# Kernel tuning notes

Hardware: AMD Instinct MI355X
Metric: run time of the kernel (lower is better)

## Reference

```python
import jax, jax.numpy as jnp
import numpy as np

N_GRAPHS = 20
NUM_GENES = 5000
N = N_GRAPHS * NUM_GENES
E = 1_600_000
F_IN = 64
H = 64
EMB = 64
L = 3  # num message-passing layers
SLOPE = 0.01  # LeakyReLU negative slope (torch default)
BN_EPS = 1e-5


def setup_inputs() -> dict:
    key = jax.random.key(0)
    ks = jax.random.split(key, 16)
    s = lambda *shape: 0.05  # init scale
    inp = {
        "x": jax.random.normal(ks[0], (N, F_IN), dtype=jnp.float32),
        "edge_index": jax.random.randint(ks[1], (2, E), 0, N, dtype=jnp.int64),
        "pre_w": jax.random.normal(ks[2], (F_IN, H), dtype=jnp.float32) * 0.05,
        "pre_b": jnp.zeros((H,), jnp.float32),
        "conv_w1": jax.random.normal(ks[3], (L, H, H), dtype=jnp.float32) * 0.05,
        "conv_b1": jnp.zeros((L, H), jnp.float32),
        "conv_w2": jax.random.normal(ks[4], (L, H, H), dtype=jnp.float32) * 0.05,
        "conv_b2": jnp.zeros((L, H), jnp.float32),
        "bn_g": jnp.ones((L - 1, H), jnp.float32),
        "bn_b": jnp.zeros((L - 1, H), jnp.float32),
        "post_w1": jax.random.normal(ks[5], (H, H), dtype=jnp.float32) * 0.05,
        "post_b1": jnp.zeros((H,), jnp.float32),
        "post_w2": jax.random.normal(ks[6], (H, EMB), dtype=jnp.float32) * 0.05,
        "post_b2": jnp.zeros((EMB,), jnp.float32),
    }
    return inp


def _gin_conv(h, src, dst, w1, b1, w2, b2):
    # GINConv(eps=0): mlp(x + sum_{j in N(i)} x_j)
    agg = jax.ops.segment_sum(h[src], dst, num_segments=N)  # [N, H]
    z = h + agg
    z = jax.nn.leaky_relu(z @ w1 + b1, negative_slope=SLOPE)
    return z @ w2 + b2


def _batchnorm(h, g, b):
    mu = jnp.mean(h, axis=0)
    var = jnp.var(h, axis=0)
    return (h - mu) * jax.lax.rsqrt(var + BN_EPS) * g + b


def reference(x, edge_index, pre_w, pre_b, conv_w1, conv_b1, conv_w2, conv_b2,
              bn_g, bn_b, post_w1, post_b1, post_w2, post_b2):
    src, dst = edge_index[0], edge_index[1]
    h = x @ pre_w + pre_b
    for l in range(L - 1):
        h = _gin_conv(h, src, dst, conv_w1[l], conv_b1[l], conv_w2[l], conv_b2[l])
        h = _batchnorm(h, bn_g[l], bn_b[l])
    h = _gin_conv(h, src, dst, conv_w1[L - 1], conv_b1[L - 1], conv_w2[L - 1], conv_b2[L - 1])
    h = jax.nn.leaky_relu(h @ post_w1 + post_b1, negative_slope=SLOPE)
    h = h @ post_w2 + post_b2  # [N, EMB]
    return h.reshape(N_GRAPHS, NUM_GENES * EMB)
```

## Files before the change

kernel.cpp:

```cpp
#include <hip/hip_runtime.h>
#include <hip/hip_bf16.h>

#define NN 100000
#define EE 1600000
#define HD 64
#define SLOPE 0.01f
#define BN_EPS 1e-5f
#define TS_BF 144
#define TS_F32 272

#define BSHIFT 9
#define BSIZE 512
#define NBUCK ((NN + BSIZE - 1) / BSIZE)
#define BCAP 16384
#define CHUNKE 8192
#define NBLKA ((EE + CHUNKE - 1) / CHUNKE)

typedef __attribute__((ext_vector_type(8))) short short8;
typedef __attribute__((ext_vector_type(8))) __bf16 bf16x8;
typedef __attribute__((ext_vector_type(4))) float f32x4;

__device__ __forceinline__ float lrelu(float v) { return v > 0.f ? v : SLOPE * v; }
__device__ __forceinline__ float bflo(unsigned u) { return __uint_as_float(u << 16); }
__device__ __forceinline__ float bfhi(unsigned u) { return __uint_as_float(u & 0xFFFF0000u); }
__device__ __forceinline__ unsigned short f2bf(float f) {
    __hip_bfloat16 hb = __float2bfloat16(f);
    return *reinterpret_cast<unsigned short*>(&hb);
}

__global__ __launch_bounds__(256) void k_binit(int* __restrict__ bcursor) {
    int t = threadIdx.x;
    if (t < NBUCK) bcursor[t] = t * BCAP;
}

__global__ __launch_bounds__(256) void k_bucketa(const int* __restrict__ src,
                                                 const int* __restrict__ dst,
                                                 int* __restrict__ bcursor,
                                                 int* __restrict__ staging) {
    __shared__ int hist[NBUCK], base_l[NBUCK], cur_l[NBUCK];
    int tid = threadIdx.x;
    int base = blockIdx.x * CHUNKE;
    int nE = min(CHUNKE, EE - base);
    for (int i = tid; i < NBUCK; i += 256) hist[i] = 0;
    __syncthreads();
    for (int k = tid; k < nE; k += 256)
        atomicAdd(&hist[dst[base + k] >> BSHIFT], 1);
    __syncthreads();
    for (int i = tid; i < NBUCK; i += 256) {
        int h = hist[i];
        base_l[i] = h ? atomicAdd(&bcursor[i], h) : 0;
        cur_l[i] = 0;
    }
    __syncthreads();
    for (int k = tid; k < nE; k += 256) {
        int d = dst[base + k];
        int s = src[base + k];
        int b = d >> BSHIFT;
        int off = atomicAdd(&cur_l[b], 1);
        staging[base_l[b] + off] = (s << BSHIFT) | (d & (BSIZE - 1));
    }
}

__global__ __launch_bounds__(256) void k_bscan(const int* __restrict__ bcursor,
                                               int* __restrict__ bbase,
                                               int* __restrict__ row_ptr) {
    __shared__ int sc[256], cnt[256];
    int tid = threadIdx.x;
    int c = (tid < NBUCK) ? (bcursor[tid] - tid * BCAP) : 0;
    cnt[tid] = c;
    sc[tid] = c;
    __syncthreads();
    for (int s = 1; s < 256; s <<= 1) {
        int v = (tid >= s) ? sc[tid - s] : 0;
        __syncthreads();
        sc[tid] += v;
        __syncthreads();
    }
    if (tid < NBUCK) bbase[tid] = sc[tid] - cnt[tid];
    if (tid == 0) row_ptr[NN] = EE;
}

__global__ __launch_bounds__(256) void k_bucketb(const int* __restrict__ staging,
                                                 const int* __restrict__ bcursor,
                                                 const int* __restrict__ bbase,
                                                 int* __restrict__ row_ptr,
                                                 int* __restrict__ csr) {
    __shared__ int cnt[BSIZE], sc[BSIZE], cur[BSIZE];
    int b = blockIdx.x, tid = threadIdx.x;
    int cnt_e = bcursor[b] - b * BCAP;
    int sbase = b * BCAP;
    int n0 = b * BSIZE;
    int nn = min(BSIZE, NN - n0);
    int bb = bbase[b];
    cnt[tid] = 0;
    cnt[tid + 256] = 0;
    __syncthreads();
    for (int i = tid; i < cnt_e; i += 256)
        atomicAdd(&cnt[staging[sbase + i] & (BSIZE - 1)], 1);
    __syncthreads();
    sc[tid] = cnt[tid];
    sc[tid + 256] = cnt[tid + 256];
    __syncthreads();
    for (int s = 1; s < BSIZE; s <<= 1) {
        int i0 = tid, i1 = tid + 256;
        int v0 = (i0 >= s) ? sc[i0 - s] : 0;
        int v1 = (i1 >= s) ? sc[i1 - s] : 0;
        __syncthreads();
        sc[i0] += v0;
        sc[i1] += v1;
        __syncthreads();
    }
    int e0 = sc[tid] - cnt[tid];
    int e1 = sc[tid + 256] - cnt[tid + 256];
    cur[tid] = e0;
    cur[tid + 256] = e1;
    if (tid < nn) row_ptr[n0 + tid] = bb + e0;
    if (tid + 256 < nn) row_ptr[n0 + tid + 256] = bb + e1;
    __syncthreads();
    for (int i = tid; i < cnt_e; i += 256) {
        int v = staging[sbase + i];
        int off = atomicAdd(&cur[v & (BSIZE - 1)], 1);
        csr[bb + off] = v >> BSHIFT;
    }
}

__global__ __launch_bounds__(256) void k_packw(const float* __restrict__ pre_w,
                                               const float* __restrict__ conv_w1,
                                               const float* __restrict__ conv_w2,
                                               const float* __restrict__ post_w1,
                                               const float* __restrict__ post_w2,
                                               unsigned short* __restrict__ wp) {
    int g = blockIdx.x >> 1;
    int c = (blockIdx.x & 1) * 256 + threadIdx.x;
    const float* W;
    switch (g) {
        case 0: W = pre_w; break;
        case 1: W = conv_w1; break;
        case 2: W = conv_w2; break;
        case 3: W = conv_w1 + 4096; break;
        case 4: W = conv_w2 + 4096; break;
        case 5: W = conv_w1 + 8192; break;
        case 6: W = conv_w2 + 8192; break;
        case 7: W = post_w1; break;
        default: W = post_w2; break;
    }
    int nt = c >> 7, ks = (c >> 6) & 1, ln = c & 63;
    int n = nt * 16 + (ln & 15);
    unsigned short* dstp = wp + (size_t)g * 4096 + (size_t)c * 8;
#pragma unroll
    for (int j = 0; j < 8; j++) {
        int k = ks * 32 + (ln >> 4) * 8 + j;
        dstp[j] = f2bf(W[k * HD + n]);
    }
}

__global__ __launch_bounds__(256, 4) void k_pre(const float* __restrict__ x,
                                                const unsigned short* __restrict__ wp0,
                                                const float* __restrict__ bias,
                                                unsigned short* __restrict__ h) {
    __shared__ char lds_all[4][16 * TS_BF];
    int tid = threadIdx.x, lane = tid & 63, wid = tid >> 6;
    int lg = lane >> 4, li = lane & 15;
    char* base = lds_all[wid];

    bf16x8 wf[4][2];
#pragma unroll
    for (int nt = 0; nt < 4; nt++)
#pragma unroll
        for (int ks = 0; ks < 2; ks++)
            wf[nt][ks] = __builtin_bit_cast(bf16x8,
                *(const short8*)(wp0 + ((size_t)((nt * 2 + ks) * 64 + lane)) * 8));
    float bb[4];
#pragma unroll
    for (int nt = 0; nt < 4; nt++) bb[nt] = bias[nt * 16 + li];

    int gwave = (blockIdx.x * 256 + tid) >> 6;
    int nwaves = (gridDim.x * 256) >> 6;
    for (int tile = gwave; tile < NN / 16; tile += nwaves) {
        int row = tile * 16 + li;
        bf16x8 af[2];
#pragma unroll
        for (int ks = 0; ks < 2; ks++) {
            const float* p = x + (size_t)row * HD + ks * 32 + lg * 8;
            union { unsigned short u[8]; short8 s; } t;
#pragma unroll
            for (int j = 0; j < 8; j++) t.u[j] = f2bf(p[j]);
            af[ks] = __builtin_bit_cast(bf16x8, t.s);
        }
        f32x4 acc[4];
#pragma unroll
        for (int nt = 0; nt < 4; nt++) acc[nt] = (f32x4){0.f, 0.f, 0.f, 0.f};
#pragma unroll
        for (int ks = 0; ks < 2; ks++)
#pragma unroll
            for (int nt = 0; nt < 4; nt++)
                acc[nt] = __builtin_amdgcn_mfma_f32_16x16x32_bf16(af[ks], wf[nt][ks], acc[nt], 0, 0, 0);
#pragma unroll
        for (int nt = 0; nt < 4; nt++)
#pragma unroll
            for (int r = 0; r < 4; r++)
                *(unsigned short*)(base + (lg * 4 + r) * TS_BF + (nt * 16 + li) * 2)
                    = f2bf(acc[nt][r] + bb[nt]);
#pragma unroll
        for (int s = 0; s < 2; s++) {
            short8 t = *(short8*)(base + li * TS_BF + (s * 4 + lg) * 16);
            *(short8*)(h + (size_t)row * HD + (s * 4 + lg) * 8) = t;
        }
    }
}

template<bool OUTF32, bool STATS>
__global__ __launch_bounds__(256, 3) void k_fmlp(const unsigned short* __restrict__ in,
                                                 const unsigned short* __restrict__ wpa,
                                                 const unsigned short* __restrict__ wpb,
                                                 const float* __restrict__ b1,
                                                 const float* __restrict__ b2,
                                                 void* __restrict__ outp,
                                                 float* __restrict__ stats_out) {
    __shared__ char lds_all[4][16 * TS_F32];
    int tid = threadIdx.x, lane = tid & 63, wid = tid >> 6;
    int lg = lane >> 4, li = lane & 15;
    char* base = lds_all[wid];

    bf16x8 w1f[4][2], w2f[4][2];
#pragma unroll
    for (int nt = 0; nt < 4; nt++)
#pragma unroll
        for (int ks = 0; ks < 2; ks++) {
            w1f[nt][ks] = __builtin_bit_cast(bf16x8,
                *(const short8*)(wpa + ((size_t)((nt * 2 + ks) * 64 + lane)) * 8));
            w2f[nt][ks] = __builtin_bit_cast(bf16x8,
                *(const short8*)(wpb + ((size_t)((nt * 2 + ks) * 64 + lane)) * 8));
        }
    float bb1[4], bb2[4];
#pragma unroll
    for (int nt = 0; nt < 4; nt++) {
        bb1[nt] = b1[nt * 16 + li];
        bb2[nt] = b2[nt * 16 + li];
    }

    float s1[4] = {0.f, 0.f, 0.f, 0.f}, s2[4] = {0.f, 0.f, 0.f, 0.f};
    int gwave = (blockIdx.x * 256 + tid) >> 6;
    int nwaves = (gridDim.x * 256) >> 6;
    for (int tile = gwave; tile < NN / 16; tile += nwaves) {
        int row = tile * 16 + li;
        bf16x8 af[2];
#pragma unroll
        for (int ks = 0; ks < 2; ks++)
            af[ks] = __builtin_bit_cast(bf16x8,
                *(const short8*)(in + (size_t)row * HD + ks * 32 + lg * 8));
        f32x4 acc[4];
#pragma unroll
        for (int nt = 0; nt < 4; nt++) acc[nt] = (f32x4){0.f, 0.f, 0.f, 0.f};
#pragma unroll
        for (int ks = 0; ks < 2; ks++)
#pragma unroll
            for (int nt = 0; nt < 4; nt++)
                acc[nt] = __builtin_amdgcn_mfma_f32_16x16x32_bf16(af[ks], w1f[nt][ks], acc[nt], 0, 0, 0);
#pragma unroll
        for (int nt = 0; nt < 4; nt++)
#pragma unroll
            for (int r = 0; r < 4; r++)
                *(unsigned short*)(base + (lg * 4 + r) * TS_BF + (nt * 16 + li) * 2)
                    = f2bf(lrelu(acc[nt][r] + bb1[nt]));
        bf16x8 a2[2];
#pragma unroll
        for (int ks = 0; ks < 2; ks++)
            a2[ks] = *(bf16x8*)(base + li * TS_BF + (ks * 32 + lg * 8) * 2);
        f32x4 acc2[4];
#pragma unroll
        for (int nt = 0; nt < 4; nt++) acc2[nt] = (f32x4){0.f, 0.f, 0.f, 0.f};
#pragma unroll
        for (int ks = 0; ks < 2; ks++)
#pragma unroll
            for (int nt = 0; nt < 4; nt++)
                acc2[nt] = __builtin_amdgcn_mfma_f32_16x16x32_bf16(a2[ks], w2f[nt][ks], acc2[nt], 0, 0, 0);
        if (OUTF32) {
#pragma unroll
            for (int nt = 0; nt < 4; nt++)
#pragma unroll
                for (int r = 0; r < 4; r++)
                    *(float*)(base + (lg * 4 + r) * TS_F32 + (nt * 16 + li) * 4)
                        = acc2[nt][r] + bb2[nt];
#pragma unroll
            for (int s = 0; s < 4; s++) {
                f32x4 t = *(f32x4*)(base + li * TS_F32 + (s * 4 + lg) * 16);
                *(f32x4*)((float*)outp + (size_t)row * HD + (s * 4 + lg) * 4) = t;
            }
        } else {
#pragma unroll
            for (int nt = 0; nt < 4; nt++) {
#pragma unroll
                for (int r = 0; r < 4; r++) {
                    float u = acc2[nt][r] + bb2[nt];
                    if (STATS) { s1[nt] += u; s2[nt] += u * u; }
                    *(unsigned short*)(base + (lg * 4 + r) * TS_BF + (nt * 16 + li) * 2)
                        = f2bf(u);
                }
            }
#pragma unroll
            for (int s = 0; s < 2; s++) {
                short8 t = *(short8*)(base + li * TS_BF + (s * 4 + lg) * 16);
                *(short8*)((unsigned short*)outp + (size_t)row * HD + (s * 4 + lg) * 8) = t;
            }
        }
    }
    if (STATS) {
#pragma unroll
        for (int nt = 0; nt < 4; nt++) {
            float a = s1[nt], b = s2[nt];
            a += __shfl_xor(a, 16); a += __shfl_xor(a, 32);
            b += __shfl_xor(b, 16); b += __shfl_xor(b, 32);
            if (lg == 0) {
                atomicAdd(&stats_out[nt * 16 + li], a);
                atomicAdd(&stats_out[64 + nt * 16 + li], b);
            }
        }
    }
}

__global__ __launch_bounds__(256, 6) void k_gather(const unsigned short* __restrict__ h,
                                                   const int* __restrict__ row_ptr,
                                                   const int* __restrict__ csr,
                                                   const float* __restrict__ bn_stats,
                                                   const float* __restrict__ bn_g,
                                                   const float* __restrict__ bn_b,
                                                   int apply_bn,
                                                   unsigned short* __restrict__ z) {
    int tid = threadIdx.x;
    int lane = tid & 63;
    int g = lane >> 4;
    int fq = lane & 15;
    int wave = (blockIdx.x * 256 + tid) >> 6;
    int node = wave * 4 + g;
    if (node >= NN) return;

    float sc[4] = {1.f, 1.f, 1.f, 1.f}, sh[4] = {0.f, 0.f, 0.f, 0.f};
    if (apply_bn) {
        float inv = 1.f / (float)NN;
#pragma unroll
        for (int j = 0; j < 4; j++) {
            int f = fq * 4 + j;
            float mu = bn_stats[f] * inv;
            float var = bn_stats[64 + f] * inv - mu * mu;
            float s = rsqrtf(var + BN_EPS) * bn_g[f];
            sc[j] = s;
            sh[j] = bn_b[f] - mu * s;
        }
    }

    const uint2* hv = (const uint2*)h;
    int r0 = row_ptr[node], re = row_ptr[node + 1];
    uint2 sv = hv[(size_t)node * 16 + fq];
    float a0[4], a1[4] = {0, 0, 0, 0}, a2[4] = {0, 0, 0, 0}, a3[4] = {0, 0, 0, 0};
    a0[0] = bflo(sv.x); a0[1] = bfhi(sv.x); a0[2] = bflo(sv.y); a0[3] = bfhi(sv.y);

    int e = r0;
    for (; e + 8 <= re; e += 8) {
        int i0 = csr[e], i1 = csr[e + 1], i2 = csr[e + 2], i3 = csr[e + 3];
        int i4 = csr[e + 4], i5 = csr[e + 5], i6 = csr[e + 6], i7 = csr[e + 7];
        uint2 v0 = hv[(size_t)i0 * 16 + fq];
        uint2 v1 = hv[(size_t)i1 * 16 + fq];
        uint2 v2 = hv[(size_t)i2 * 16 + fq];
        uint2 v3 = hv[(size_t)i3 * 16 + fq];
        uint2 v4 = hv[(size_t)i4 * 16 + fq];
        uint2 v5 = hv[(size_t)i5 * 16 + fq];
        uint2 v6 = hv[(size_t)i6 * 16 + fq];
        uint2 v7 = hv[(size_t)i7 * 16 + fq];
        a0[0] += bflo(v0.x); a0[1] += bfhi(v0.x); a0[2] += bflo(v0.y); a0[3] += bfhi(v0.y);
        a1[0] += bflo(v1.x); a1[1] += bfhi(v1.x); a1[2] += bflo(v1.y); a1[3] += bfhi(v1.y);
        a2[0] += bflo(v2.x); a2[1] += bfhi(v2.x); a2[2] += bflo(v2.y); a2[3] += bfhi(v2.y);
        a3[0] += bflo(v3.x); a3[1] += bfhi(v3.x); a3[2] += bflo(v3.y); a3[3] += bfhi(v3.y);
        a0[0] += bflo(v4.x); a0[1] += bfhi(v4.x); a0[2] += bflo(v4.y); a0[3] += bfhi(v4.y);
        a1[0] += bflo(v5.x); a1[1] += bfhi(v5.x); a1[2] += bflo(v5.y); a1[3] += bfhi(v5.y);
        a2[0] += bflo(v6.x); a2[1] += bfhi(v6.x); a2[2] += bflo(v6.y); a2[3] += bfhi(v6.y);
        a3[0] += bflo(v7.x); a3[1] += bfhi(v7.x); a3[2] += bflo(v7.y); a3[3] += bfhi(v7.y);
    }
    for (; e < re; e++) {
        uint2 v = hv[(size_t)csr[e] * 16 + fq];
        a0[0] += bflo(v.x); a0[1] += bfhi(v.x); a0[2] += bflo(v.y); a0[3] += bfhi(v.y);
    }
    float cnt = (float)(re - r0 + 1);
    unsigned short o[4];
#pragma unroll
    for (int j = 0; j < 4; j++) {
        float s = ((a0[j] + a1[j]) + (a2[j] + a3[j]));
        if (apply_bn) s = fmaf(s, sc[j], cnt * sh[j]);
        o[j] = f2bf(s);
    }
    uint2 ov;
    ov.x = (unsigned)o[0] | ((unsigned)o[1] << 16);
    ov.y = (unsigned)o[2] | ((unsigned)o[3] << 16);
    ((uint2*)z)[(size_t)node * 16 + fq] = ov;
}

extern "C" void kernel_launch(void* const* d_in, const int* in_sizes, int n_in,
                              void* d_out, int out_size, void* d_ws, size_t ws_size,
                              hipStream_t stream) {
    const float* x = (const float*)d_in[0];
    const int* edge = (const int*)d_in[1];
    const float* pre_w = (const float*)d_in[2];
    const float* pre_b = (const float*)d_in[3];
    const float* conv_w1 = (const float*)d_in[4];
    const float* conv_b1 = (const float*)d_in[5];
    const float* conv_w2 = (const float*)d_in[6];
    const float* conv_b2 = (const float*)d_in[7];
    const float* bn_g = (const float*)d_in[8];
    const float* bn_b = (const float*)d_in[9];
    const float* post_w1 = (const float*)d_in[10];
    const float* post_b1 = (const float*)d_in[11];
    const float* post_w2 = (const float*)d_in[12];
    const float* post_b2 = (const float*)d_in[13];
    float* out = (float*)d_out;

    const int* src = edge;
    const int* dst = edge + EE;

    unsigned short* hH = (unsigned short*)d_ws;
    unsigned short* zZ = hH + (size_t)NN * HD;
    float* stats0 = (float*)(zZ + (size_t)NN * HD);
    float* stats1 = stats0 + 128;
    unsigned short* wp = (unsigned short*)(stats1 + 128);
    int* row_ptr = (int*)(wp + 9 * 4096);
    int* csr = row_ptr + NN + 4;
    int* bcursor = csr + EE;
    int* bbase = bcursor + 256;
    int* staging = bbase + 256;

    dim3 blk(256);
    dim3 gG(6250), gM(782);

    hipMemsetAsync(stats0, 0, 256 * sizeof(float), stream);
    hipLaunchKernelGGL(k_binit, dim3(1), blk, 0, stream, bcursor);
    hipLaunchKernelGGL(k_bucketa, dim3(NBLKA), blk, 0, stream, src, dst, bcursor, staging);
    hipLaunchKernelGGL(k_bscan, dim3(1), blk, 0, stream, bcursor, bbase, row_ptr);
    hipLaunchKernelGGL(k_bucketb, dim3(NBUCK), blk, 0, stream, staging, bcursor, bbase,
                       row_ptr, csr);

    hipLaunchKernelGGL(k_packw, dim3(18), blk, 0, stream,
                       pre_w, conv_w1, conv_w2, post_w1, post_w2, wp);

    hipLaunchKernelGGL(k_pre, gM, blk, 0, stream, x, wp + 0 * 4096, pre_b, hH);

    hipLaunchKernelGGL(k_gather, gG, blk, 0, stream, hH, row_ptr, csr,
                       (const float*)nullptr, (const float*)nullptr, (const float*)nullptr, 0, zZ);
    hipLaunchKernelGGL((k_fmlp<false, true>), gM, blk, 0, stream, zZ,
                       wp + 1 * 4096, wp + 2 * 4096, conv_b1, conv_b2, (void*)hH, stats0);

    hipLaunchKernelGGL(k_gather, gG, blk, 0, stream, hH, row_ptr, csr,
                       stats0, bn_g, bn_b, 1, zZ);
    hipLaunchKernelGGL((k_fmlp<false, true>), gM, blk, 0, stream, zZ,
                       wp + 3 * 4096, wp + 4 * 4096, conv_b1 + HD, conv_b2 + HD, (void*)hH, stats1);

    hipLaunchKernelGGL(k_gather, gG, blk, 0, stream, hH, row_ptr, csr,
                       stats1, bn_g + HD, bn_b + HD, 1, zZ);
    hipLaunchKernelGGL((k_fmlp<false, false>), gM, blk, 0, stream, zZ,
                       wp + 5 * 4096, wp + 6 * 4096, conv_b1 + 2 * HD, conv_b2 + 2 * HD,
                       (void*)hH, stats0);

    hipLaunchKernelGGL((k_fmlp<true, false>), gM, blk, 0, stream, hH,
                       wp + 7 * 4096, wp + 8 * 4096, post_b1, post_b2, (void*)out, stats0);
}
```

Before: 375.4 us.

## Fuse neighbor gather with GIN MLP into a single per-tile kernel

Merges the edge-gather aggregation (with BatchNorm folding) and the two-layer GIN MLP into one kernel, where each wave gathers 16 nodes into LDS and then runs the MFMA MLP on them. This removes the intermediate z buffer round-trip through global memory and three kernel launches. Ping-pong buffers replace the in-place h/z pair, and the post MLP is split into its own kernel. The trade-off is fewer concurrent waves for the latency-bound gather and heavier register use per wave.

```diff
diff --git a/kernel.cpp b/kernel.cpp
--- a/kernel.cpp
+++ b/kernel.cpp
@@ -8,6 +8,7 @@
 #define BN_EPS 1e-5f
 #define TS_BF 144
 #define TS_F32 272
+#define NTILE (NN / 16)
 
 #define BSHIFT 9
 #define BSIZE 512
@@ -176,7 +177,7 @@
 
     int gwave = (blockIdx.x * 256 + tid) >> 6;
     int nwaves = (gridDim.x * 256) >> 6;
-    for (int tile = gwave; tile < NN / 16; tile += nwaves) {
+    for (int tile = gwave; tile < NTILE; tile += nwaves) {
         int row = tile * 16 + li;
         bf16x8 af[2];
 #pragma unroll
@@ -209,18 +210,26 @@
     }
 }
 
-template<bool OUTF32, bool STATS>
-__global__ __launch_bounds__(256, 3) void k_fmlp(const unsigned short* __restrict__ in,
-                                                 const unsigned short* __restrict__ wpa,
-                                                 const unsigned short* __restrict__ wpb,
-                                                 const float* __restrict__ b1,
-                                                 const float* __restrict__ b2,
-                                                 void* __restrict__ outp,
-                                                 float* __restrict__ stats_out) {
-    __shared__ char lds_all[4][16 * TS_F32];
+template<bool APPLY_BN, bool STATS>
+__global__ __launch_bounds__(256, 4) void k_gfmlp(const unsigned short* __restrict__ h,
+                                                  const int* __restrict__ row_ptr,
+                                                  const int* __restrict__ csr,
+                                                  const float* __restrict__ bn_stats,
+                                                  const float* __restrict__ bn_g,
+                                                  const float* __restrict__ bn_b,
+                                                  const unsigned short* __restrict__ wpa,
+                                                  const unsigned short* __restrict__ wpb,
+                                                  const float* __restrict__ b1,
+                                                  const float* __restrict__ b2,
+                                                  unsigned short* __restrict__ outp,
+                                                  float* __restrict__ stats_out) {
+    __shared__ char lds_all[4][16 * TS_BF];
     int tid = threadIdx.x, lane = tid & 63, wid = tid >> 6;
     int lg = lane >> 4, li = lane & 15;
     char* base = lds_all[wid];
+
+    int tile = (blockIdx.x * 256 + tid) >> 6;
+    if (tile >= NTILE) return;
 
     bf16x8 w1f[4][2], w2f[4][2];
 #pragma unroll
@@ -239,71 +248,113 @@
         bb2[nt] = b2[nt * 16 + li];
     }
 
+    float sc[4], sh[4];
+    if (APPLY_BN) {
+        float inv = 1.f / (float)NN;
+#pragma unroll
+        for (int j = 0; j < 4; j++) {
+            int f = li * 4 + j;
+            float mu = bn_stats[f] * inv;
+            float var = bn_stats[64 + f] * inv - mu * mu;
+            float s = rsqrtf(var + BN_EPS) * bn_g[f];
+            sc[j] = s;
+            sh[j] = bn_b[f] - mu * s;
+        }
+    }
+
+    const uint2* hv = (const uint2*)h;
+#pragma unroll
+    for (int b = 0; b < 4; b++) {
+        int node = tile * 16 + b * 4 + lg;
+        int r0 = row_ptr[node], re = row_ptr[node + 1];
+        uint2 sv = hv[(size_t)node * 16 + li];
+        float a0[4], a1[4] = {0, 0, 0, 0}, a2[4] = {0, 0, 0, 0}, a3[4] = {0, 0, 0, 0};
+        a0[0] = bflo(sv.x); a0[1] = bfhi(sv.x); a0[2] = bflo(sv.y); a0[3] = bfhi(sv.y);
+        int e = r0;
+        for (; e + 8 <= re; e += 8) {
+            int i0 = csr[e], i1 = csr[e + 1], i2 = csr[e + 2], i3 = csr[e + 3];
+            int i4 = csr[e + 4], i5 = csr[e + 5], i6 = csr[e + 6], i7 = csr[e + 7];
+            uint2 v0 = hv[(size_t)i0 * 16 + li];
+            uint2 v1 = hv[(size_t)i1 * 16 + li];
+            uint2 v2 = hv[(size_t)i2 * 16 + li];
+            uint2 v3 = hv[(size_t)i3 * 16 + li];
+            uint2 v4 = hv[(size_t)i4 * 16 + li];
+            uint2 v5 = hv[(size_t)i5 * 16 + li];
+            uint2 v6 = hv[(size_t)i6 * 16 + li];
+            uint2 v7 = hv[(size_t)i7 * 16 + li];
+            a0[0] += bflo(v0.x); a0[1] += bfhi(v0.x); a0[2] += bflo(v0.y); a0[3] += bfhi(v0.y);
+            a1[0] += bflo(v1.x); a1[1] += bfhi(v1.x); a1[2] += bflo(v1.y); a1[3] += bfhi(v1.y);
+            a2[0] += bflo(v2.x); a2[1] += bfhi(v2.x); a2[2] += bflo(v2.y); a2[3] += bfhi(v2.y);
+            a3[0] += bflo(v3.x); a3[1] += bfhi(v3.x); a3[2] += bflo(v3.y); a3[3] += bfhi(v3.y);
+            a0[0] += bflo(v4.x); a0[1] += bfhi(v4.x); a0[2] += bflo(v4.y); a0[3] += bfhi(v4.y);
+            a1[0] += bflo(v5.x); a1[1] += bfhi(v5.x); a1[2] += bflo(v5.y); a1[3] += bfhi(v5.y);
+            a2[0] += bflo(v6.x); a2[1] += bfhi(v6.x); a2[2] += bflo(v6.y); a2[3] += bfhi(v6.y);
+            a3[0] += bflo(v7.x); a3[1] += bfhi(v7.x); a3[2] += bflo(v7.y); a3[3] += bfhi(v7.y);
+        }
+        for (; e < re; e++) {
+            uint2 v = hv[(size_t)csr[e] * 16 + li];
+            a0[0] += bflo(v.x); a0[1] += bfhi(v.x); a0[2] += bflo(v.y); a0[3] += bfhi(v.y);
+        }
+        float cnt = (float)(re - r0 + 1);
+        unsigned short o[4];
+#pragma unroll
+        for (int j = 0; j < 4; j++) {
+            float s = ((a0[j] + a1[j]) + (a2[j] + a3[j]));
+            if (APPLY_BN) s = fmaf(s, sc[j], cnt * sh[j]);
+            o[j] = f2bf(s);
+        }
+        uint2 ov;
+        ov.x = (unsigned)o[0] | ((unsigned)o[1] << 16);
+        ov.y = (unsigned)o[2] | ((unsigned)o[3] << 16);
+        *(uint2*)(base + (b * 4 + lg) * TS_BF + li * 8) = ov;
+    }
+
+    bf16x8 af[2];
+#pragma unroll
+    for (int ks = 0; ks < 2; ks++)
+        af[ks] = *(bf16x8*)(base + li * TS_BF + (ks * 32 + lg * 8) * 2);
+    f32x4 acc[4];
+#pragma unroll
+    for (int nt = 0; nt < 4; nt++) acc[nt] = (f32x4){0.f, 0.f, 0.f, 0.f};
+#pragma unroll
+    for (int ks = 0; ks < 2; ks++)
+#pragma unroll
+        for (int nt = 0; nt < 4; nt++)
+            acc[nt] = __builtin_amdgcn_mfma_f32_16x16x32_bf16(af[ks], w1f[nt][ks], acc[nt], 0, 0, 0);
+#pragma unroll
+    for (int nt = 0; nt < 4; nt++)
+#pragma unroll
+        for (int r = 0; r < 4; r++)
+            *(unsigned short*)(base + (lg * 4 + r) * TS_BF + (nt * 16 + li) * 2)
+                = f2bf(lrelu(acc[nt][r] + bb1[nt]));
+    bf16x8 a2f[2];
+#pragma unroll
+    for (int ks = 0; ks < 2; ks++)
+        a2f[ks] = *(bf16x8*)(base + li * TS_BF + (ks * 32 + lg * 8) * 2);
+    f32x4 acc2[4];
+#pragma unroll
+    for (int nt = 0; nt < 4; nt++) acc2[nt] = (f32x4){0.f, 0.f, 0.f, 0.f};
+#pragma unroll
+    for (int ks = 0; ks < 2; ks++)
+#pragma unroll
+        for (int nt = 0; nt < 4; nt++)
+            acc2[nt] = __builtin_amdgcn_mfma_f32_16x16x32_bf16(a2f[ks], w2f[nt][ks], acc2[nt], 0, 0, 0);
+
     float s1[4] = {0.f, 0.f, 0.f, 0.f}, s2[4] = {0.f, 0.f, 0.f, 0.f};
-    int gwave = (blockIdx.x * 256 + tid) >> 6;
-    int nwaves = (gridDim.x * 256) >> 6;
-    for (int tile = gwave; tile < NN / 16; tile += nwaves) {
-        int row = tile * 16 + li;
-        bf16x8 af[2];
-#pragma unroll
-        for (int ks = 0; ks < 2; ks++)
-            af[ks] = __builtin_bit_cast(bf16x8,
-                *(const short8*)(in + (size_t)row * HD + ks * 32 + lg * 8));
-        f32x4 acc[4];
-#pragma unroll
-        for (int nt = 0; nt < 4; nt++) acc[nt] = (f32x4){0.f, 0.f, 0.f, 0.f};
-#pragma unroll
-        for (int ks = 0; ks < 2; ks++)
-#pragma unroll
-            for (int nt = 0; nt < 4; nt++)
-                acc[nt] = __builtin_amdgcn_mfma_f32_16x16x32_bf16(af[ks], w1f[nt][ks], acc[nt], 0, 0, 0);
-#pragma unroll
-        for (int nt = 0; nt < 4; nt++)
-#pragma unroll
-            for (int r = 0; r < 4; r++)
-                *(unsigned short*)(base + (lg * 4 + r) * TS_BF + (nt * 16 + li) * 2)
-                    = f2bf(lrelu(acc[nt][r] + bb1[nt]));
-        bf16x8 a2[2];
-#pragma unroll
-        for (int ks = 0; ks < 2; ks++)
-            a2[ks] = *(bf16x8*)(base + li * TS_BF + (ks * 32 + lg * 8) * 2);
-        f32x4 acc2[4];
-#pragma unroll
-        for (int nt = 0; nt < 4; nt++) acc2[nt] = (f32x4){0.f, 0.f, 0.f, 0.f};
-#pragma unroll
-        for (int ks = 0; ks < 2; ks++)
-#pragma unroll
-            for (int nt = 0; nt < 4; nt++)
-                acc2[nt] = __builtin_amdgcn_mfma_f32_16x16x32_bf16(a2[ks], w2f[nt][ks], acc2[nt], 0, 0, 0);
-        if (OUTF32) {
-#pragma unroll
-            for (int nt = 0; nt < 4; nt++)
-#pragma unroll
-                for (int r = 0; r < 4; r++)
-                    *(float*)(base + (lg * 4 + r) * TS_F32 + (nt * 16 + li) * 4)
-                        = acc2[nt][r] + bb2[nt];
-#pragma unroll
-            for (int s = 0; s < 4; s++) {
-                f32x4 t = *(f32x4*)(base + li * TS_F32 + (s * 4 + lg) * 16);
-                *(f32x4*)((float*)outp + (size_t)row * HD + (s * 4 + lg) * 4) = t;
-            }
-        } else {
-#pragma unroll
-            for (int nt = 0; nt < 4; nt++) {
-#pragma unroll
-                for (int r = 0; r < 4; r++) {
-                    float u = acc2[nt][r] + bb2[nt];
-                    if (STATS) { s1[nt] += u; s2[nt] += u * u; }
-                    *(unsigned short*)(base + (lg * 4 + r) * TS_BF + (nt * 16 + li) * 2)
-                        = f2bf(u);
-                }
-            }
-#pragma unroll
-            for (int s = 0; s < 2; s++) {
-                short8 t = *(short8*)(base + li * TS_BF + (s * 4 + lg) * 16);
-                *(short8*)((unsigned short*)outp + (size_t)row * HD + (s * 4 + lg) * 8) = t;
-            }
-        }
+#pragma unroll
+    for (int nt = 0; nt < 4; nt++) {
+#pragma unroll
+        for (int r = 0; r < 4; r++) {
+            float u = acc2[nt][r] + bb2[nt];
+            if (STATS) { s1[nt] += u; s2[nt] += u * u; }
+            *(unsigned short*)(base + (lg * 4 + r) * TS_BF + (nt * 16 + li) * 2) = f2bf(u);
+        }
+    }
+    int row = tile * 16 + li;
+#pragma unroll
+    for (int s = 0; s < 2; s++) {
+        short8 t = *(short8*)(base + li * TS_BF + (s * 4 + lg) * 16);
+        *(short8*)(outp + (size_t)row * HD + (s * 4 + lg) * 8) = t;
     }
     if (STATS) {
 #pragma unroll
@@ -319,79 +370,81 @@
     }
 }
 
-__global__ __launch_bounds__(256, 6) void k_gather(const unsigned short* __restrict__ h,
-                                                   const int* __restrict__ row_ptr,
-                                                   const int* __restrict__ csr,
-                                                   const float* __restrict__ bn_stats,
-                                                   const float* __restrict__ bn_g,
-                                                   const float* __restrict__ bn_b,
-                                                   int apply_bn,
-                                                   unsigned short* __restrict__ z) {
-    int tid = threadIdx.x;
-    int lane = tid & 63;
-    int g = lane >> 4;
-    int fq = lane & 15;
-    int wave = (blockIdx.x * 256 + tid) >> 6;
-    int node = wave * 4 + g;
-    if (node >= NN) return;
-
-    float sc[4] = {1.f, 1.f, 1.f, 1.f}, sh[4] = {0.f, 0.f, 0.f, 0.f};
-    if (apply_bn) {
-        float inv = 1.f / (float)NN;
-#pragma unroll
-        for (int j = 0; j < 4; j++) {
-            int f = fq * 4 + j;
-            float mu = bn_stats[f] * inv;
-            float var = bn_stats[64 + f] * inv - mu * mu;
-            float s = rsqrtf(var + BN_EPS) * bn_g[f];
-            sc[j] = s;
-            sh[j] = bn_b[f] - mu * s;
-        }
-    }
-
-    const uint2* hv = (const uint2*)h;
-    int r0 = row_ptr[node], re = row_ptr[node + 1];
-    uint2 sv = hv[(size_t)node * 16 + fq];
-    float a0[4], a1[4] = {0, 0, 0, 0}, a2[4] = {0, 0, 0, 0}, a3[4] = {0, 0, 0, 0};
-    a0[0] = bflo(sv.x); a0[1] = bfhi(sv.x); a0[2] = bflo(sv.y); a0[3] = bfhi(sv.y);
-
-    int e = r0;
-    for (; e + 8 <= re; e += 8) {
-        int i0 = csr[e], i1 = csr[e + 1], i2 = csr[e + 2], i3 = csr[e + 3];
-        int i4 = csr[e + 4], i5 = csr[e + 5], i6 = csr[e + 6], i7 = csr[e + 7];
-        uint2 v0 = hv[(size_t)i0 * 16 + fq];
-        uint2 v1 = hv[(size_t)i1 * 16 + fq];
-        uint2 v2 = hv[(size_t)i2 * 16 + fq];
-        uint2 v3 = hv[(size_t)i3 * 16 + fq];
-        uint2 v4 = hv[(size_t)i4 * 16 + fq];
-        uint2 v5 = hv[(size_t)i5 * 16 + fq];
-        uint2 v6 = hv[(size_t)i6 * 16 + fq];
-        uint2 v7 = hv[(size_t)i7 * 16 + fq];
-        a0[0] += bflo(v0.x); a0[1] += bfhi(v0.x); a0[2] += bflo(v0.y); a0[3] += bfhi(v0.y);
-        a1[0] += bflo(v1.x); a1[1] += bfhi(v1.x); a1[2] += bflo(v1.y); a1[3] += bfhi(v1.y);
-        a2[0] += bflo(v2.x); a2[1] += bfhi(v2.x); a2[2] += bflo(v2.y); a2[3] += bfhi(v2.y);
-        a3[0] += bflo(v3.x); a3[1] += bfhi(v3.x); a3[2] += bflo(v3.y); a3[3] += bfhi(v3.y);
-        a0[0] += bflo(v4.x); a0[1] += bfhi(v4.x); a0[2] += bflo(v4.y); a0[3] += bfhi(v4.y);
-        a1[0] += bflo(v5.x); a1[1] += bfhi(v5.x); a1[2] += bflo(v5.y); a1[3] += bfhi(v5.y);
-        a2[0] += bflo(v6.x); a2[1] += bfhi(v6.x); a2[2] += bflo(v6.y); a2[3] += bfhi(v6.y);
-        a3[0] += bflo(v7.x); a3[1] += bfhi(v7.x); a3[2] += bflo(v7.y); a3[3] += bfhi(v7.y);
-    }
-    for (; e < re; e++) {
-        uint2 v = hv[(size_t)csr[e] * 16 + fq];
-        a0[0] += bflo(v.x); a0[1] += bfhi(v.x); a0[2] += bflo(v.y); a0[3] += bfhi(v.y);
-    }
-    float cnt = (float)(re - r0 + 1);
-    unsigned short o[4];
-#pragma unroll
-    for (int j = 0; j < 4; j++) {
-        float s = ((a0[j] + a1[j]) + (a2[j] + a3[j]));
-        if (apply_bn) s = fmaf(s, sc[j], cnt * sh[j]);
-        o[j] = f2bf(s);
-    }
-    uint2 ov;
-    ov.x = (unsigned)o[0] | ((unsigned)o[1] << 16);
-    ov.y = (unsigned)o[2] | ((unsigned)o[3] << 16);
-    ((uint2*)z)[(size_t)node * 16 + fq] = ov;
+__global__ __launch_bounds__(256, 3) void k_post(const unsigned short* __restrict__ in,
+                                                 const unsigned short* __restrict__ wpa,
+                                                 const unsigned short* __restrict__ wpb,
+                                                 const float* __restrict__ b1,
+                                                 const float* __restrict__ b2,
+                                                 float* __restrict__ outp) {
+    __shared__ char lds_all[4][16 * TS_F32];
+    int tid = threadIdx.x, lane = tid & 63, wid = tid >> 6;
+    int lg = lane >> 4, li = lane & 15;
+    char* base = lds_all[wid];
+
+    bf16x8 w1f[4][2], w2f[4][2];
+#pragma unroll
+    for (int nt = 0; nt < 4; nt++)
+#pragma unroll
+        for (int ks = 0; ks < 2; ks++) {
+            w1f[nt][ks] = __builtin_bit_cast(bf16x8,
+                *(const short8*)(wpa + ((size_t)((nt * 2 + ks) * 64 + lane)) * 8));
+            w2f[nt][ks] = __builtin_bit_cast(bf16x8,
+                *(const short8*)(wpb + ((size_t)((nt * 2 + ks) * 64 + lane)) * 8));
+        }
+    float bb1[4], bb2[4];
+#pragma unroll
+    for (int nt = 0; nt < 4; nt++) {
+        bb1[nt] = b1[nt * 16 + li];
+        bb2[nt] = b2[nt * 16 + li];
+    }
+
+    int gwave = (blockIdx.x * 256 + tid) >> 6;
+    int nwaves = (gridDim.x * 256) >> 6;
+    for (int tile = gwave; tile < NTILE; tile += nwaves) {
+        int row = tile * 16 + li;
+        bf16x8 af[2];
+#pragma unroll
+        for (int ks = 0; ks < 2; ks++)
+            af[ks] = __builtin_bit_cast(bf16x8,
+                *(const short8*)(in + (size_t)row * HD + ks * 32 + lg * 8));
+        f32x4 acc[4];
+#pragma unroll
+        for (int nt = 0; nt < 4; nt++) acc[nt] = (f32x4){0.f, 0.f, 0.f, 0.f};
+#pragma unroll
+        for (int ks = 0; ks < 2; ks++)
+#pragma unroll
+            for (int nt = 0; nt < 4; nt++)
+                acc[nt] = __builtin_amdgcn_mfma_f32_16x16x32_bf16(af[ks], w1f[nt][ks], acc[nt], 0, 0, 0);
+#pragma unroll
+        for (int nt = 0; nt < 4; nt++)
+#pragma unroll
+            for (int r = 0; r < 4; r++)
+                *(unsigned short*)(base + (lg * 4 + r) * TS_BF + (nt * 16 + li) * 2)
+                    = f2bf(lrelu(acc[nt][r] + bb1[nt]));
+        bf16x8 a2[2];
+#pragma unroll
+        for (int ks = 0; ks < 2; ks++)
+            a2[ks] = *(bf16x8*)(base + li * TS_BF + (ks * 32 + lg * 8) * 2);
+        f32x4 acc2[4];
+#pragma unroll
+        for (int nt = 0; nt < 4; nt++) acc2[nt] = (f32x4){0.f, 0.f, 0.f, 0.f};
+#pragma unroll
+        for (int ks = 0; ks < 2; ks++)
+#pragma unroll
+            for (int nt = 0; nt < 4; nt++)
+                acc2[nt] = __builtin_amdgcn_mfma_f32_16x16x32_bf16(a2[ks], w2f[nt][ks], acc2[nt], 0, 0, 0);
+#pragma unroll
+        for (int nt = 0; nt < 4; nt++)
+#pragma unroll
+            for (int r = 0; r < 4; r++)
+                *(float*)(base + (lg * 4 + r) * TS_F32 + (nt * 16 + li) * 4)
+                    = acc2[nt][r] + bb2[nt];
+#pragma unroll
+        for (int s = 0; s < 4; s++) {
+            f32x4 t = *(f32x4*)(base + li * TS_F32 + (s * 4 + lg) * 16);
+            *(f32x4*)(outp + (size_t)row * HD + (s * 4 + lg) * 4) = t;
+        }
+    }
 }
 
 extern "C" void kernel_launch(void* const* d_in, const int* in_sizes, int n_in,
@@ -416,9 +469,9 @@
     const int* src = edge;
     const int* dst = edge + EE;
 
-    unsigned short* hH = (unsigned short*)d_ws;
-    unsigned short* zZ = hH + (size_t)NN * HD;
-    float* stats0 = (float*)(zZ + (size_t)NN * HD);
+    unsigned short* hA = (unsigned short*)d_ws;
+    unsigned short* hB = hA + (size_t)NN * HD;
+    float* stats0 = (float*)(hB + (size_t)NN * HD);
     float* stats1 = stats0 + 128;
     unsigned short* wp = (unsigned short*)(stats1 + 128);
     int* row_ptr = (int*)(wp + 9 * 4096);
@@ -428,7 +481,8 @@
     int* staging = bbase + 256;
 
     dim3 blk(256);
-    dim3 gG(6250), gM(782);
+    dim3 gLoop(782);
+    dim3 gFused(1563);
 
     hipMemsetAsync(stats0, 0, 256 * sizeof(float), stream);
     hipLaunchKernelGGL(k_binit, dim3(1), blk, 0, stream, bcursor);
@@ -440,24 +494,21 @@
     hipLaunchKernelGGL(k_packw, dim3(18), blk, 0, stream,
                        pre_w, conv_w1, conv_w2, post_w1, post_w2, wp);
 
-    hipLaunchKernelGGL(k_pre, gM, blk, 0, stream, x, wp + 0 * 4096, pre_b, hH);
-
-    hipLaunchKernelGGL(k_gather, gG, blk, 0, stream, hH, row_ptr, csr,
-                       (const float*)nullptr, (const float*)nullptr, (const float*)nullptr, 0, zZ);
-    hipLaunchKernelGGL((k_fmlp<false, true>), gM, blk, 0, stream, zZ,
-                       wp + 1 * 4096, wp + 2 * 4096, conv_b1, conv_b2, (void*)hH, stats0);
-
-    hipLaunchKernelGGL(k_gather, gG, blk, 0, stream, hH, row_ptr, csr,
-                       stats0, bn_g, bn_b, 1, zZ);
-    hipLaunchKernelGGL((k_fmlp<false, true>), gM, blk, 0, stream, zZ,
-                       wp + 3 * 4096, wp + 4 * 4096, conv_b1 + HD, conv_b2 + HD, (void*)hH, stats1);
-
-    hipLaunchKernelGGL(k_gather, gG, blk, 0, stream, hH, row_ptr, csr,
-                       stats1, bn_g + HD, bn_b + HD, 1, zZ);
-    hipLaunchKernelGGL((k_fmlp<false, false>), gM, blk, 0, stream, zZ,
+    hipLaunchKernelGGL(k_pre, gLoop, blk, 0, stream, x, wp + 0 * 4096, pre_b, hA);
+
+    hipLaunchKernelGGL((k_gfmlp<false, true>), gFused, blk, 0, stream, hA, row_ptr, csr,
+                       (const float*)nullptr, (const float*)nullptr, (const float*)nullptr,
+                       wp + 1 * 4096, wp + 2 * 4096, conv_b1, conv_b2, hB, stats0);
+
+    hipLaunchKernelGGL((k_gfmlp<true, true>), gFused, blk, 0, stream, hB, row_ptr, csr,
+                       stats0, bn_g, bn_b,
+                       wp + 3 * 4096, wp + 4 * 4096, conv_b1 + HD, conv_b2 + HD, hA, stats1);
+
+    hipLaunchKernelGGL((k_gfmlp<true, false>), gFused, blk, 0, stream, hA, row_ptr, csr,
+                       stats1, bn_g + HD, bn_b + HD,
                        wp + 5 * 4096, wp + 6 * 4096, conv_b1 + 2 * HD, conv_b2 + 2 * HD,
-                       (void*)hH, stats0);
-
-    hipLaunchKernelGGL((k_fmlp<true, false>), gM, blk, 0, stream, hH,
-                       wp + 7 * 4096, wp + 8 * 4096, post_b1, post_b2, (void*)out, stats0);
-}
+                       hB, stats0);
+
+    hipLaunchKernelGGL(k_post, gLoop, blk, 0, stream, hB,
+                       wp + 7 * 4096, wp + 8 * 4096, post_b1, post_b2, out);
+}
```

Result: slower. 522.0 us (+39.0%).
